# Kernel tuning notes

Measured on AMD Instinct MI355X. Metric: run time of the kernel, lower is better.

Reference implementation:

```python
import jax, jax.numpy as jnp
import numpy as np

DIM_CODES = 512
DICT_SIZE = 512
EMBED_DIM = 16
BATCH = 512


def setup_inputs() -> dict:
    key = jax.random.key(0)
    k1, k2 = jax.random.split(key)
    mu = jax.random.normal(k1, (BATCH, DIM_CODES * EMBED_DIM), dtype=jnp.float32)
    dictionary = jax.random.normal(k2, (DIM_CODES, DICT_SIZE, EMBED_DIM), dtype=jnp.float32)
    return {"mu": mu, "dictionary": dictionary}


def reference(mu, dictionary):
    # mu: [B, C*E], dictionary: [C, K, E]
    B = mu.shape[0]
    C, K, E = dictionary.shape
    mu3 = mu.reshape(B, C, E)
    # pairwise squared distance ||mu - d||^2 = ||mu||^2 + ||d||^2 - 2 mu.d -> [B, C, K]
    dist = (jnp.sum(mu3 * mu3, axis=-1)[..., None]
            + jnp.sum(dictionary * dictionary, axis=-1)[None]
            - 2.0 * jnp.einsum('bce,cke->bck', mu3, dictionary))
    idx = jnp.argmin(dist, axis=-1)  # [B, C] int
    # gather nearest codebook entries: per-code index into its own codebook
    z_embed = dictionary[jnp.arange(C)[None, :], idx]  # [B, C, E]
    z_embed = z_embed.reshape(B, C * E)
    # TransferGrad: forward = z_embed, backward passes grad straight-through to mu
    z = mu + jax.lax.stop_gradient(z_embed - mu)
    one_hot_idx = jax.nn.one_hot(idx, K, dtype=mu.dtype)  # [B, C, K]
    return z, z_embed, one_hot_idx
```

## Files before the change

kernel.cpp:

```cpp
#include <hip/hip_runtime.h>
#include <float.h>

constexpr int C    = 512;
constexpr int K    = 512;
constexpr int E    = 16;
constexpr int B    = 512;
constexpr int ROWS = 128;
constexpr int MUS  = C * E;

__launch_bounds__(256, 2)
__global__ void vq_kernel(const float* __restrict__ mu,
                          const float* __restrict__ dict,
                          float* __restrict__ z,
                          float* __restrict__ zq,
                          float* __restrict__ oh)
{
    const int c    = blockIdx.x;
    const int b0   = blockIdx.y * ROWS;
    const int tid  = threadIdx.x;
    const int lane = tid & 63;
    const int wave = tid >> 6;

    __shared__ float mu_s[ROWS][E];

    const float* __restrict__ dbase = dict + (size_t)c * K * E;

    float4 dv[8][4];
    float  nrm[8];
#pragma unroll
    for (int i = 0; i < 8; ++i) {
        const int k = lane + 64 * i;
        const float4* p = reinterpret_cast<const float4*>(dbase + k * E);
        dv[i][0] = p[0]; dv[i][1] = p[1]; dv[i][2] = p[2]; dv[i][3] = p[3];
        float s = dv[i][0].x * dv[i][0].x;
        s = fmaf(dv[i][0].y, dv[i][0].y, s);
        s = fmaf(dv[i][0].z, dv[i][0].z, s);
        s = fmaf(dv[i][0].w, dv[i][0].w, s);
#pragma unroll
        for (int t = 1; t < 4; ++t) {
            s = fmaf(dv[i][t].x, dv[i][t].x, s);
            s = fmaf(dv[i][t].y, dv[i][t].y, s);
            s = fmaf(dv[i][t].z, dv[i][t].z, s);
            s = fmaf(dv[i][t].w, dv[i][t].w, s);
        }
        nrm[i] = s;
    }

    {
        const int r = tid >> 2, q = tid & 3;
#pragma unroll
        for (int rep = 0; rep < 2; ++rep) {
            const int row = r + rep * 64;
            const float4* p = reinterpret_cast<const float4*>(
                mu + (size_t)(b0 + row) * MUS + c * E);
            reinterpret_cast<float4*>(&mu_s[row][0])[q] = p[q];
        }
    }
    __syncthreads();

    for (int j = 0; j < ROWS / 4; ++j) {
        const int bl = wave + 4 * j;
        const int b  = b0 + bl;

        float4 m[4];
#pragma unroll
        for (int t = 0; t < 4; ++t)
            m[t] = reinterpret_cast<const float4*>(&mu_s[bl][0])[t];

        float nmu = m[0].x * m[0].x;
        nmu = fmaf(m[0].y, m[0].y, nmu);
        nmu = fmaf(m[0].z, m[0].z, nmu);
        nmu = fmaf(m[0].w, m[0].w, nmu);
#pragma unroll
        for (int t = 1; t < 4; ++t) {
            nmu = fmaf(m[t].x, m[t].x, nmu);
            nmu = fmaf(m[t].y, m[t].y, nmu);
            nmu = fmaf(m[t].z, m[t].z, nmu);
            nmu = fmaf(m[t].w, m[t].w, nmu);
        }

        float dist_v[8];
        float best_d = FLT_MAX;
        int   best_k = K;
#pragma unroll
        for (int i = 0; i < 8; ++i) {
            float acc = dv[i][0].x * m[0].x;
            acc = fmaf(dv[i][0].y, m[0].y, acc);
            acc = fmaf(dv[i][0].z, m[0].z, acc);
            acc = fmaf(dv[i][0].w, m[0].w, acc);
#pragma unroll
            for (int t = 1; t < 4; ++t) {
                acc = fmaf(dv[i][t].x, m[t].x, acc);
                acc = fmaf(dv[i][t].y, m[t].y, acc);
                acc = fmaf(dv[i][t].z, m[t].z, acc);
                acc = fmaf(dv[i][t].w, m[t].w, acc);
            }
            const float dist = fmaf(-2.0f, acc, nmu + nrm[i]);
            dist_v[i] = dist;
            const int k = lane + 64 * i;
            if (dist < best_d) { best_d = dist; best_k = k; }
        }

#pragma unroll
        for (int off = 32; off; off >>= 1) {
            const float od = __shfl_down(best_d, off);
            const int   ok = __shfl_down(best_k, off);
            if (od < best_d || (od == best_d && ok < best_k)) {
                best_d = od; best_k = ok;
            }
        }
        best_k = __shfl(best_k, 0);
        best_d = __shfl(best_d, 0);

        float sec = FLT_MAX;
#pragma unroll
        for (int i = 0; i < 8; ++i) {
            const int k = lane + 64 * i;
            sec = (k != best_k) ? fminf(sec, dist_v[i]) : sec;
        }
#pragma unroll
        for (int off = 32; off; off >>= 1)
            sec = fminf(sec, __shfl_down(sec, off));
        sec = __shfl(sec, 0);

        if (sec - best_d < 1e-3f) {
            double nmuD = 0.0;
#pragma unroll
            for (int t = 0; t < 4; ++t) {
                nmuD += (double)m[t].x * m[t].x + (double)m[t].y * m[t].y
                      + (double)m[t].z * m[t].z + (double)m[t].w * m[t].w;
            }
            double bd = DBL_MAX;
            int    bk = K;
#pragma unroll
            for (int i = 0; i < 8; ++i) {
                double nd = 0.0, dt = 0.0;
#pragma unroll
                for (int t = 0; t < 4; ++t) {
                    nd += (double)dv[i][t].x * dv[i][t].x
                        + (double)dv[i][t].y * dv[i][t].y
                        + (double)dv[i][t].z * dv[i][t].z
                        + (double)dv[i][t].w * dv[i][t].w;
                    dt += (double)dv[i][t].x * m[t].x
                        + (double)dv[i][t].y * m[t].y
                        + (double)dv[i][t].z * m[t].z
                        + (double)dv[i][t].w * m[t].w;
                }
                const double dist = nmuD + nd - 2.0 * dt;
                const int k = lane + 64 * i;
                if (dist < bd) { bd = dist; bk = k; }
            }
#pragma unroll
            for (int off = 32; off; off >>= 1) {
                const double od = __shfl_down(bd, off);
                const int    ok = __shfl_down(bk, off);
                if (od < bd || (od == bd && ok < bk)) { bd = od; bk = ok; }
            }
            best_k = __shfl(bk, 0);
        }

        float* ohp = oh + ((size_t)b * C + c) * K;
#pragma unroll
        for (int h = 0; h < 2; ++h) {
            const int kb = h * 256 + lane * 4;
            float4 v;
            v.x = (kb + 0 == best_k) ? 1.0f : 0.0f;
            v.y = (kb + 1 == best_k) ? 1.0f : 0.0f;
            v.z = (kb + 2 == best_k) ? 1.0f : 0.0f;
            v.w = (kb + 3 == best_k) ? 1.0f : 0.0f;
            *reinterpret_cast<float4*>(ohp + kb) = v;
        }

        if (lane < E) {
            const float dq = dbase[best_k * E + lane];
            const float mm = mu_s[bl][lane];
            const size_t o = (size_t)b * MUS + (size_t)c * E + lane;
            zq[o] = dq;
            z[o]  = mm + (dq - mm);
        }
    }
}

extern "C" void kernel_launch(void* const* d_in, const int* in_sizes, int n_in,
                              void* d_out, int out_size, void* d_ws, size_t ws_size,
                              hipStream_t stream)
{
    const float* mu   = (const float*)d_in[0];
    const float* dict = (const float*)d_in[1];

    float* z  = (float*)d_out;
    float* zq = z  + (size_t)B * C * E;
    float* oh = zq + (size_t)B * C * E;

    dim3 grid(C, B / ROWS);
    vq_kernel<<<grid, 256, 0, stream>>>(mu, dict, z, zq, oh);
}
```

Before: 696.3 us.

## Process two rows per wave, use ballot-based argmin and nontemporal stores

Each wave now handles two batch rows per iteration, interleaving their butterfly min reductions for more ILP. The per-lane second-best distance is tracked inline, and the argmin lane is found with a ballot instead of a paired value/index shuffle reduction plus a second pass over distances. Output writes (one-hot, z, zq) use nontemporal stores to reduce cache pollution on the large, store-dominated output. Register pressure rises with two rows in flight, and tie-breaking relies on the lowest lane holding the minimum.

```diff
diff --git a/kernel.cpp b/kernel.cpp
--- a/kernel.cpp
+++ b/kernel.cpp
@@ -7,6 +7,8 @@
 constexpr int B    = 512;
 constexpr int ROWS = 128;
 constexpr int MUS  = C * E;
+
+typedef float f32x4 __attribute__((ext_vector_type(4)));
 
 __launch_bounds__(256, 2)
 __global__ void vq_kernel(const float* __restrict__ mu,
@@ -58,125 +60,133 @@
     }
     __syncthreads();
 
-    for (int j = 0; j < ROWS / 4; ++j) {
-        const int bl = wave + 4 * j;
-        const int b  = b0 + bl;
-
-        float4 m[4];
-#pragma unroll
-        for (int t = 0; t < 4; ++t)
-            m[t] = reinterpret_cast<const float4*>(&mu_s[bl][0])[t];
-
-        float nmu = m[0].x * m[0].x;
-        nmu = fmaf(m[0].y, m[0].y, nmu);
-        nmu = fmaf(m[0].z, m[0].z, nmu);
-        nmu = fmaf(m[0].w, m[0].w, nmu);
-#pragma unroll
-        for (int t = 1; t < 4; ++t) {
-            nmu = fmaf(m[t].x, m[t].x, nmu);
-            nmu = fmaf(m[t].y, m[t].y, nmu);
-            nmu = fmaf(m[t].z, m[t].z, nmu);
-            nmu = fmaf(m[t].w, m[t].w, nmu);
-        }
-
-        float dist_v[8];
-        float best_d = FLT_MAX;
-        int   best_k = K;
-#pragma unroll
-        for (int i = 0; i < 8; ++i) {
-            float acc = dv[i][0].x * m[0].x;
-            acc = fmaf(dv[i][0].y, m[0].y, acc);
-            acc = fmaf(dv[i][0].z, m[0].z, acc);
-            acc = fmaf(dv[i][0].w, m[0].w, acc);
+    for (int j = 0; j < ROWS / 8; ++j) {
+        int    bl[2];
+        float4 m[2][4];
+        float  nmu[2], bd[2], sec[2];
+        int    bk[2];
+
+#pragma unroll
+        for (int pr = 0; pr < 2; ++pr) {
+            bl[pr] = wave + 8 * j + 4 * pr;
+
+#pragma unroll
+            for (int t = 0; t < 4; ++t)
+                m[pr][t] = reinterpret_cast<const float4*>(&mu_s[bl[pr]][0])[t];
+
+            float nm = m[pr][0].x * m[pr][0].x;
+            nm = fmaf(m[pr][0].y, m[pr][0].y, nm);
+            nm = fmaf(m[pr][0].z, m[pr][0].z, nm);
+            nm = fmaf(m[pr][0].w, m[pr][0].w, nm);
 #pragma unroll
             for (int t = 1; t < 4; ++t) {
-                acc = fmaf(dv[i][t].x, m[t].x, acc);
-                acc = fmaf(dv[i][t].y, m[t].y, acc);
-                acc = fmaf(dv[i][t].z, m[t].z, acc);
-                acc = fmaf(dv[i][t].w, m[t].w, acc);
-            }
-            const float dist = fmaf(-2.0f, acc, nmu + nrm[i]);
-            dist_v[i] = dist;
-            const int k = lane + 64 * i;
-            if (dist < best_d) { best_d = dist; best_k = k; }
-        }
-
+                nm = fmaf(m[pr][t].x, m[pr][t].x, nm);
+                nm = fmaf(m[pr][t].y, m[pr][t].y, nm);
+                nm = fmaf(m[pr][t].z, m[pr][t].z, nm);
+                nm = fmaf(m[pr][t].w, m[pr][t].w, nm);
+            }
+            nmu[pr] = nm;
+
+            float bdl = FLT_MAX, secl = FLT_MAX;
+            int   bkl = K;
+#pragma unroll
+            for (int i = 0; i < 8; ++i) {
+                float acc = dv[i][0].x * m[pr][0].x;
+                acc = fmaf(dv[i][0].y, m[pr][0].y, acc);
+                acc = fmaf(dv[i][0].z, m[pr][0].z, acc);
+                acc = fmaf(dv[i][0].w, m[pr][0].w, acc);
+#pragma unroll
+                for (int t = 1; t < 4; ++t) {
+                    acc = fmaf(dv[i][t].x, m[pr][t].x, acc);
+                    acc = fmaf(dv[i][t].y, m[pr][t].y, acc);
+                    acc = fmaf(dv[i][t].z, m[pr][t].z, acc);
+                    acc = fmaf(dv[i][t].w, m[pr][t].w, acc);
+                }
+                const float dist = fmaf(-2.0f, acc, nm + nrm[i]);
+                const int   k    = lane + 64 * i;
+                const bool  lt   = dist < bdl;
+                secl = lt ? bdl : fminf(secl, dist);
+                bdl  = lt ? dist : bdl;
+                bkl  = lt ? k : bkl;
+            }
+            bd[pr] = bdl; sec[pr] = secl; bk[pr] = bkl;
+        }
+
+        float w0 = bd[0], w1 = bd[1];
 #pragma unroll
         for (int off = 32; off; off >>= 1) {
-            const float od = __shfl_down(best_d, off);
-            const int   ok = __shfl_down(best_k, off);
-            if (od < best_d || (od == best_d && ok < best_k)) {
-                best_d = od; best_k = ok;
-            }
-        }
-        best_k = __shfl(best_k, 0);
-        best_d = __shfl(best_d, 0);
-
-        float sec = FLT_MAX;
-#pragma unroll
-        for (int i = 0; i < 8; ++i) {
-            const int k = lane + 64 * i;
-            sec = (k != best_k) ? fminf(sec, dist_v[i]) : sec;
-        }
-#pragma unroll
-        for (int off = 32; off; off >>= 1)
-            sec = fminf(sec, __shfl_down(sec, off));
-        sec = __shfl(sec, 0);
-
-        if (sec - best_d < 1e-3f) {
-            double nmuD = 0.0;
-#pragma unroll
-            for (int t = 0; t < 4; ++t) {
-                nmuD += (double)m[t].x * m[t].x + (double)m[t].y * m[t].y
-                      + (double)m[t].z * m[t].z + (double)m[t].w * m[t].w;
-            }
-            double bd = DBL_MAX;
-            int    bk = K;
-#pragma unroll
-            for (int i = 0; i < 8; ++i) {
-                double nd = 0.0, dt = 0.0;
+            w0 = fminf(w0, __shfl_xor(w0, off));
+            w1 = fminf(w1, __shfl_xor(w1, off));
+        }
+        const float w[2] = { w0, w1 };
+
+#pragma unroll
+        for (int pr = 0; pr < 2; ++pr) {
+            const int bl_ = bl[pr];
+            const int b   = b0 + bl_;
+
+            const unsigned long long mask = __ballot(bd[pr] == w[pr]);
+            const int lane0 = __ffsll(mask) - 1;
+            int best_k = __shfl(bk[pr], lane0);
+
+            const float cand = (lane == lane0) ? sec[pr] : bd[pr];
+            if (__any(cand < w[pr] + 1e-3f)) {
+                double nmuD = 0.0;
 #pragma unroll
                 for (int t = 0; t < 4; ++t) {
-                    nd += (double)dv[i][t].x * dv[i][t].x
-                        + (double)dv[i][t].y * dv[i][t].y
-                        + (double)dv[i][t].z * dv[i][t].z
-                        + (double)dv[i][t].w * dv[i][t].w;
-                    dt += (double)dv[i][t].x * m[t].x
-                        + (double)dv[i][t].y * m[t].y
-                        + (double)dv[i][t].z * m[t].z
-                        + (double)dv[i][t].w * m[t].w;
-                }
-                const double dist = nmuD + nd - 2.0 * dt;
-                const int k = lane + 64 * i;
-                if (dist < bd) { bd = dist; bk = k; }
-            }
-#pragma unroll
-            for (int off = 32; off; off >>= 1) {
-                const double od = __shfl_down(bd, off);
-                const int    ok = __shfl_down(bk, off);
-                if (od < bd || (od == bd && ok < bk)) { bd = od; bk = ok; }
-            }
-            best_k = __shfl(bk, 0);
-        }
-
-        float* ohp = oh + ((size_t)b * C + c) * K;
-#pragma unroll
-        for (int h = 0; h < 2; ++h) {
-            const int kb = h * 256 + lane * 4;
-            float4 v;
-            v.x = (kb + 0 == best_k) ? 1.0f : 0.0f;
-            v.y = (kb + 1 == best_k) ? 1.0f : 0.0f;
-            v.z = (kb + 2 == best_k) ? 1.0f : 0.0f;
-            v.w = (kb + 3 == best_k) ? 1.0f : 0.0f;
-            *reinterpret_cast<float4*>(ohp + kb) = v;
-        }
-
-        if (lane < E) {
-            const float dq = dbase[best_k * E + lane];
-            const float mm = mu_s[bl][lane];
-            const size_t o = (size_t)b * MUS + (size_t)c * E + lane;
-            zq[o] = dq;
-            z[o]  = mm + (dq - mm);
+                    nmuD += (double)m[pr][t].x * m[pr][t].x
+                          + (double)m[pr][t].y * m[pr][t].y
+                          + (double)m[pr][t].z * m[pr][t].z
+                          + (double)m[pr][t].w * m[pr][t].w;
+                }
+                double bD = DBL_MAX;
+                int    bK = K;
+#pragma unroll
+                for (int i = 0; i < 8; ++i) {
+                    double nd = 0.0, dt = 0.0;
+#pragma unroll
+                    for (int t = 0; t < 4; ++t) {
+                        nd += (double)dv[i][t].x * dv[i][t].x
+                            + (double)dv[i][t].y * dv[i][t].y
+                            + (double)dv[i][t].z * dv[i][t].z
+                            + (double)dv[i][t].w * dv[i][t].w;
+                        dt += (double)dv[i][t].x * m[pr][t].x
+                            + (double)dv[i][t].y * m[pr][t].y
+                            + (double)dv[i][t].z * m[pr][t].z
+                            + (double)dv[i][t].w * m[pr][t].w;
+                    }
+                    const double dist = nmuD + nd - 2.0 * dt;
+                    const int k = lane + 64 * i;
+                    if (dist < bD) { bD = dist; bK = k; }
+                }
+#pragma unroll
+                for (int off = 32; off; off >>= 1) {
+                    const double od = __shfl_down(bD, off);
+                    const int    ok = __shfl_down(bK, off);
+                    if (od < bD || (od == bD && ok < bK)) { bD = od; bK = ok; }
+                }
+                best_k = __shfl(bK, 0);
+            }
+
+            float* ohp = oh + ((size_t)b * C + c) * K;
+#pragma unroll
+            for (int h = 0; h < 2; ++h) {
+                const int kb = h * 256 + lane * 4;
+                f32x4 v;
+                v.x = (kb + 0 == best_k) ? 1.0f : 0.0f;
+                v.y = (kb + 1 == best_k) ? 1.0f : 0.0f;
+                v.z = (kb + 2 == best_k) ? 1.0f : 0.0f;
+                v.w = (kb + 3 == best_k) ? 1.0f : 0.0f;
+                __builtin_nontemporal_store(v, reinterpret_cast<f32x4*>(ohp + kb));
+            }
+
+            if (lane < E) {
+                const float dq = dbase[best_k * E + lane];
+                const float mm = mu_s[bl_][lane];
+                const size_t o = (size_t)b * MUS + (size_t)c * E + lane;
+                __builtin_nontemporal_store(dq, zq + o);
+                __builtin_nontemporal_store(mm + (dq - mm), z + o);
+            }
         }
     }
 }
```

Result: slower. 1.029 ms (+47.8%).

## Software-pipeline row compute with emit and track second-best per lane

Applied to the files above, without the earlier changes.

Splits the per-row work into a compute step and an emit step, then software-pipelines them so the distance computation for the next row overlaps the reductions and one-hot stores of the previous row. Each lane now keeps both its local best and its second-best distance, which removes the stored dist_v array and the second cross-lane pass. The winning lane is found with an xor-shuffle min plus a ballot. The double-precision tie check now fires when any lane's candidate falls within the threshold. This adds register pressure and reloads mu from LDS in the fallback path.

```diff
diff --git a/kernel.cpp b/kernel.cpp
--- a/kernel.cpp
+++ b/kernel.cpp
@@ -58,30 +58,26 @@
     }
     __syncthreads();
 
-    for (int j = 0; j < ROWS / 4; ++j) {
-        const int bl = wave + 4 * j;
-        const int b  = b0 + bl;
-
+    auto compute_row = [&](int bl, float& obd, float& osec, int& obk) {
         float4 m[4];
 #pragma unroll
         for (int t = 0; t < 4; ++t)
             m[t] = reinterpret_cast<const float4*>(&mu_s[bl][0])[t];
 
-        float nmu = m[0].x * m[0].x;
-        nmu = fmaf(m[0].y, m[0].y, nmu);
-        nmu = fmaf(m[0].z, m[0].z, nmu);
-        nmu = fmaf(m[0].w, m[0].w, nmu);
+        float nm = m[0].x * m[0].x;
+        nm = fmaf(m[0].y, m[0].y, nm);
+        nm = fmaf(m[0].z, m[0].z, nm);
+        nm = fmaf(m[0].w, m[0].w, nm);
 #pragma unroll
         for (int t = 1; t < 4; ++t) {
-            nmu = fmaf(m[t].x, m[t].x, nmu);
-            nmu = fmaf(m[t].y, m[t].y, nmu);
-            nmu = fmaf(m[t].z, m[t].z, nmu);
-            nmu = fmaf(m[t].w, m[t].w, nmu);
-        }
-
-        float dist_v[8];
-        float best_d = FLT_MAX;
-        int   best_k = K;
+            nm = fmaf(m[t].x, m[t].x, nm);
+            nm = fmaf(m[t].y, m[t].y, nm);
+            nm = fmaf(m[t].z, m[t].z, nm);
+            nm = fmaf(m[t].w, m[t].w, nm);
+        }
+
+        float bdl = FLT_MAX, secl = FLT_MAX;
+        int   bkl = K;
 #pragma unroll
         for (int i = 0; i < 8; ++i) {
             float acc = dv[i][0].x * m[0].x;
@@ -95,43 +91,39 @@
                 acc = fmaf(dv[i][t].z, m[t].z, acc);
                 acc = fmaf(dv[i][t].w, m[t].w, acc);
             }
-            const float dist = fmaf(-2.0f, acc, nmu + nrm[i]);
-            dist_v[i] = dist;
-            const int k = lane + 64 * i;
-            if (dist < best_d) { best_d = dist; best_k = k; }
-        }
-
-#pragma unroll
-        for (int off = 32; off; off >>= 1) {
-            const float od = __shfl_down(best_d, off);
-            const int   ok = __shfl_down(best_k, off);
-            if (od < best_d || (od == best_d && ok < best_k)) {
-                best_d = od; best_k = ok;
-            }
-        }
-        best_k = __shfl(best_k, 0);
-        best_d = __shfl(best_d, 0);
-
-        float sec = FLT_MAX;
-#pragma unroll
-        for (int i = 0; i < 8; ++i) {
-            const int k = lane + 64 * i;
-            sec = (k != best_k) ? fminf(sec, dist_v[i]) : sec;
-        }
+            const float dist = fmaf(-2.0f, acc, nm + nrm[i]);
+            const int   k    = lane + 64 * i;
+            const bool  lt   = dist < bdl;
+            secl = lt ? bdl : fminf(secl, dist);
+            bdl  = lt ? dist : bdl;
+            bkl  = lt ? k : bkl;
+        }
+        obd = bdl; osec = secl; obk = bkl;
+    };
+
+    auto emit_row = [&](int bl_, float bd, float sec, int bk) {
+        const int b = b0 + bl_;
+
+        float w = bd;
 #pragma unroll
         for (int off = 32; off; off >>= 1)
-            sec = fminf(sec, __shfl_down(sec, off));
-        sec = __shfl(sec, 0);
-
-        if (sec - best_d < 1e-3f) {
+            w = fminf(w, __shfl_xor(w, off));
+
+        const unsigned long long mask = __ballot(bd == w);
+        const int lane0 = __ffsll(mask) - 1;
+        int best_k = __shfl(bk, lane0);
+
+        const float cand = (lane == lane0) ? sec : bd;
+        if (__any(cand < w + 1e-3f)) {
+            float mf[E];
+#pragma unroll
+            for (int t = 0; t < E; ++t) mf[t] = mu_s[bl_][t];
             double nmuD = 0.0;
 #pragma unroll
-            for (int t = 0; t < 4; ++t) {
-                nmuD += (double)m[t].x * m[t].x + (double)m[t].y * m[t].y
-                      + (double)m[t].z * m[t].z + (double)m[t].w * m[t].w;
-            }
-            double bd = DBL_MAX;
-            int    bk = K;
+            for (int t = 0; t < E; ++t) nmuD += (double)mf[t] * mf[t];
+
+            double bD = DBL_MAX;
+            int    bK = K;
 #pragma unroll
             for (int i = 0; i < 8; ++i) {
                 double nd = 0.0, dt = 0.0;
@@ -141,22 +133,22 @@
                         + (double)dv[i][t].y * dv[i][t].y
                         + (double)dv[i][t].z * dv[i][t].z
                         + (double)dv[i][t].w * dv[i][t].w;
-                    dt += (double)dv[i][t].x * m[t].x
-                        + (double)dv[i][t].y * m[t].y
-                        + (double)dv[i][t].z * m[t].z
-                        + (double)dv[i][t].w * m[t].w;
+                    dt += (double)dv[i][t].x * mf[4 * t + 0]
+                        + (double)dv[i][t].y * mf[4 * t + 1]
+                        + (double)dv[i][t].z * mf[4 * t + 2]
+                        + (double)dv[i][t].w * mf[4 * t + 3];
                 }
                 const double dist = nmuD + nd - 2.0 * dt;
                 const int k = lane + 64 * i;
-                if (dist < bd) { bd = dist; bk = k; }
+                if (dist < bD) { bD = dist; bK = k; }
             }
 #pragma unroll
             for (int off = 32; off; off >>= 1) {
-                const double od = __shfl_down(bd, off);
-                const int    ok = __shfl_down(bk, off);
-                if (od < bd || (od == bd && ok < bk)) { bd = od; bk = ok; }
+                const double od = __shfl_down(bD, off);
+                const int    ok = __shfl_down(bK, off);
+                if (od < bD || (od == bD && ok < bK)) { bD = od; bK = ok; }
             }
-            best_k = __shfl(bk, 0);
+            best_k = __shfl(bK, 0);
         }
 
         float* ohp = oh + ((size_t)b * C + c) * K;
@@ -173,11 +165,28 @@
 
         if (lane < E) {
             const float dq = dbase[best_k * E + lane];
-            const float mm = mu_s[bl][lane];
+            const float mm = mu_s[bl_][lane];
             const size_t o = (size_t)b * MUS + (size_t)c * E + lane;
             zq[o] = dq;
             z[o]  = mm + (dq - mm);
         }
+    };
+
+    {
+        int   pbl = wave;
+        float pbd, psec;
+        int   pbk;
+        compute_row(pbl, pbd, psec, pbk);
+
+        for (int j = 1; j < ROWS / 4; ++j) {
+            const int cbl = wave + 4 * j;
+            float cbd, csec;
+            int   cbk;
+            compute_row(cbl, cbd, csec, cbk);
+            emit_row(pbl, pbd, psec, pbk);
+            pbl = cbl; pbd = cbd; psec = csec; pbk = cbk;
+        }
+        emit_row(pbl, pbd, psec, pbk);
     }
 }
 
```

Result: slower. 751.1 us (+7.9%).
